# Performance work log

Measured on AMD Instinct MI355X. Metric: run time of the kernel, lower is better.

Reference implementation:

```python
import jax, jax.numpy as jnp
import numpy as np

N, F, H, C = 4096, 128, 32, 205   # nodes, in-features, hidden=32, clusters=ceil(4096/20)
L, T, R = 512, 12, 4              # teams, team size, replaced members per team
EPS_POOL = 1e-15                  # torch_geometric EPS in dense_diff_pool
BN_EPS = 1e-5


def setup_inputs():
    ks = jax.random.split(jax.random.key(0), 12)
    rng = np.random.default_rng(0)
    # distinct node ids per team; replace = first R members, remain = rest
    teams = np.argsort(rng.random((L, N)), axis=1)[:, :T].astype(np.int64)
    g = lambda i, shape, s: jax.random.normal(ks[i], shape, jnp.float32) * s
    D = 2 * H + C  # 269
    return {
        'x': g(0, (N, F), 1.0),
        'adj': jax.random.uniform(ks[1], (1, N, N), jnp.float32),
        'sample_teams': jnp.asarray(teams),
        'sample_replaces': jnp.asarray(teams[:, :R]),
        'W1r': g(2, (F, H), 0.08), 'b1': jnp.zeros((H,), jnp.float32), 'W1root': g(3, (F, H), 0.08),
        'g1': jnp.ones((H,), jnp.float32), 'be1': jnp.zeros((H,), jnp.float32),
        'W2r': g(4, (H, H), 0.17), 'b2': jnp.zeros((H,), jnp.float32), 'W2root': g(5, (H, H), 0.17),
        'g2': jnp.ones((H,), jnp.float32), 'be2': jnp.zeros((H,), jnp.float32),
        'W3r': g(6, (H, C), 0.17), 'b3': jnp.zeros((C,), jnp.float32), 'W3root': g(7, (H, C), 0.17),
        'g3': jnp.ones((C,), jnp.float32), 'be3': jnp.zeros((C,), jnp.float32),
        'Wl1': g(8, (D, C), 0.07), 'bl1': jnp.zeros((C,), jnp.float32),
    }


def _conv(x, adj, Wr, br, Wroot):
    # DenseGraphConv: lin_rel(adj @ x) + lin_root(x)  (lin_root has no bias)
    return jnp.matmul(adj, x) @ Wr + br + x @ Wroot


def _bn(x, gamma, beta):
    # BatchNorm1d in training mode over flattened (B*N, C)
    B, n, c = x.shape
    xf = x.reshape(-1, c)
    m = xf.mean(0)
    v = jnp.mean((xf - m) ** 2, axis=0)  # biased variance, as torch uses for normalization
    return (((xf - m) / jnp.sqrt(v + BN_EPS)) * gamma + beta).reshape(B, n, c)


def _rownorm(a, eps=1e-8):
    n = jnp.linalg.norm(a, axis=1, keepdims=True)
    return a / jnp.maximum(n, eps)


def reference(x, adj, sample_teams, sample_replaces, W1r, b1, W1root, g1, be1,
              W2r, b2, W2root, g2, be2, W3r, b3, W3root, g3, be3, Wl1, bl1):
    # GNN tower (relu before bn, matching self.bn(i, conv(...).relu()))
    x1 = _bn(jax.nn.relu(_conv(x, adj, W1r, b1, W1root)), g1, be1)    # [1,N,H]
    x2 = _bn(jax.nn.relu(_conv(x1, adj, W2r, b2, W2root)), g2, be2)   # [1,N,H]
    x3 = _bn(jax.nn.relu(_conv(x2, adj, W3r, b3, W3root)), g3, be3)   # [1,N,C]
    xcat = jnp.concatenate([x1, x2, x3], axis=-1)                     # [1,N,2H+C]
    s1 = jax.nn.softmax(jax.nn.relu(xcat @ Wl1 + bl1), axis=2)        # [1,N,C]

    # link-prediction style norm: || s1[0] @ s1[0]^T - adj ||_F
    tmp = s1[0] @ s1[0].T - adj                                       # [1,N,N]
    norm = jnp.sqrt(jnp.sum(tmp * tmp))

    # dense_diff_pool entropy loss (it re-softmaxes its input s)
    s2 = jax.nn.softmax(s1, axis=-1)
    e1 = jnp.mean(jnp.sum(-s2 * jnp.log(s2 + EPS_POOL), axis=-1))

    # similarity alignment: only the diagonal of sim_matrix(sim_x_mat, sim_s_mat) is summed
    xn = _rownorm(x)
    sn = _rownorm(s1[0])
    sim_x_mat = xn @ xn.T                                             # [N,N]
    sim_s_mat = sn @ sn.T                                             # [N,N]
    a_n = _rownorm(sim_x_mat)
    b_n = _rownorm(sim_s_mat)
    sim = -jnp.sum(a_n * b_n) / sim_x_mat.shape[0]

    # per-team replace/remain mean-embedding L1 loss (padded segment means)
    emb = xcat[0]                                                     # [N, 2H+C]
    rep = emb[sample_replaces].mean(axis=1)                           # [L, D]
    rem = emb[sample_teams[:, R:]].mean(axis=1)                       # [L, D]
    embedding_loss = jnp.mean(jnp.sum(jnp.abs(rep - rem), axis=-1))

    total_loss = 100.0 * norm + 10.0 * e1 + 100.0 * sim + embedding_loss
    return (s1, norm, e1, sim, total_loss, embedding_loss, emb)
```

## Files before the change

### kernel.cpp

```cpp
#include <hip/hip_runtime.h>
#include <math.h>

#define NN 4096
#define FF 128
#define HH 32
#define CC 205
#define DD 269
#define LL 512
#define TT 12
#define RR 4
#define GP 208
#define DP 288
#define BST 40
#define GTS 224
#define SC(i) ((i) * 32)

typedef __attribute__((ext_vector_type(8))) short bf16x8;
typedef __attribute__((ext_vector_type(4))) float f32x4;
typedef __attribute__((ext_vector_type(8))) unsigned short u16x8;

__device__ __forceinline__ float wave_sum(float v) {
#pragma unroll
  for (int o = 32; o > 0; o >>= 1) v += __shfl_xor(v, o, 64);
  return v;
}
__device__ __forceinline__ float wave_max(float v) {
#pragma unroll
  for (int o = 32; o > 0; o >>= 1) v = fmaxf(v, __shfl_xor(v, o, 64));
  return v;
}
__device__ __forceinline__ unsigned short f2bf(float x) {
  union { float f; unsigned u; } v; v.f = x;
  unsigned r = v.u + 0x7FFFu + ((v.u >> 16) & 1u);
  return (unsigned short)(r >> 16);
}

__global__ __launch_bounds__(256) void k_prep(const float* __restrict__ x,
                                              const float* __restrict__ W1r,
                                              const float* __restrict__ W1root,
                                              const float* __restrict__ Wl1,
                                              unsigned short* __restrict__ mB,
                                              float* __restrict__ rootb,
                                              float* __restrict__ xn,
                                              unsigned short* __restrict__ xnR,
                                              unsigned short* __restrict__ xnB,
                                              unsigned short* __restrict__ Wl1T) {
  __shared__ float sX[32][132];
  __shared__ unsigned short sT[32][34];
  __shared__ unsigned short sT2[FF][34];
  const int tid = threadIdx.x;
  {
    const int i = blockIdx.x * 256 + tid;
    if (i < GP * DP) {
      const int c = i / DP, k = i - c * DP;
      Wl1T[i] = (c < CC && k < DD) ? f2bf(Wl1[(size_t)k * CC + c]) : (unsigned short)0;
    }
  }
  if (blockIdx.x < 128) {
    const int kb = blockIdx.x;
    for (int p = tid; p < 1024; p += 256) {
      const int node = p >> 5, c4 = p & 31;
      const float4 v = *reinterpret_cast<const float4*>(&x[((size_t)(kb * 32 + node)) * FF + c4 * 4]);
      sX[node][c4 * 4 + 0] = v.x; sX[node][c4 * 4 + 1] = v.y;
      sX[node][c4 * 4 + 2] = v.z; sX[node][c4 * 4 + 3] = v.w;
    }
    __syncthreads();
    const int c = tid & 31, g = tid >> 5;
    float a1[4] = {0.f, 0.f, 0.f, 0.f}, a2[4] = {0.f, 0.f, 0.f, 0.f};
    for (int k = 0; k < FF; ++k) {
      const float w1 = W1r[k * HH + c];
      const float w2 = W1root[k * HH + c];
#pragma unroll
      for (int ni = 0; ni < 4; ++ni) {
        const float av = sX[g * 4 + ni][k];
        a1[ni] = fmaf(av, w1, a1[ni]);
        a2[ni] = fmaf(av, w2, a2[ni]);
      }
    }
#pragma unroll
    for (int ni = 0; ni < 4; ++ni) {
      rootb[((size_t)kb * 32 + g * 4 + ni) * HH + c] = a2[ni];
      sT[c][g * 4 + ni] = f2bf(a1[ni]);
    }
    __syncthreads();
    if (tid < 128) {
      const int row = tid >> 2, seg = tid & 3;
      u16x8 v;
#pragma unroll
      for (int j = 0; j < 8; ++j) v[j] = sT[row][seg * 8 + j];
      *reinterpret_cast<u16x8*>(&mB[((size_t)kb * 32 + row) * 32 + seg * 8]) = v;
    }
  } else {
    const int kb = blockIdx.x - 128;
    const int lane = tid & 63;
    const int w = tid >> 6;
#pragma unroll
    for (int i = 0; i < 8; ++i) {
      const int node = w * 8 + i;
      const int row = kb * 32 + node;
      const float v0 = x[(size_t)row * FF + lane];
      const float v1 = x[(size_t)row * FF + 64 + lane];
      const float ss = wave_sum(v0 * v0 + v1 * v1);
      const float n = fmaxf(sqrtf(ss), 1e-8f);
      const float a = v0 / n, b = v1 / n;
      xn[(size_t)row * FF + lane] = a;
      xn[(size_t)row * FF + 64 + lane] = b;
      xnR[(size_t)row * FF + lane] = f2bf(a);
      xnR[(size_t)row * FF + 64 + lane] = f2bf(b);
      sT2[lane][node] = f2bf(a);
      sT2[64 + lane][node] = f2bf(b);
    }
    __syncthreads();
    const int rowc = tid >> 1, seg = (tid & 1) * 16;
    if (rowc < FF) {
      u16x8 a, b;
#pragma unroll
      for (int j = 0; j < 8; ++j) { a[j] = sT2[rowc][seg + j]; b[j] = sT2[rowc][seg + 8 + j]; }
      *reinterpret_cast<u16x8*>(&xnB[((size_t)kb * GP + rowc) * 32 + seg]) = a;
      *reinterpret_cast<u16x8*>(&xnB[((size_t)kb * GP + rowc) * 32 + seg + 8]) = b;
    }
  }
}

__global__ __launch_bounds__(512) void k_conv1(const float* __restrict__ adj,
                                               unsigned short* __restrict__ adj_t,
                                               const unsigned short* __restrict__ mB,
                                               const float* __restrict__ bias,
                                               const float* __restrict__ root,
                                               float* __restrict__ t,
                                               float* __restrict__ colsum,
                                               float* __restrict__ colsq,
                                               float* __restrict__ scalars) {
  __shared__ unsigned short sA[16][520];
  __shared__ float sRed[8][16][33];
  __shared__ float ls[HH], lq[HH];
  __shared__ float redsq[8];
  const int tid = threadIdx.x;
  const int lane = tid & 63;
  const int w = tid >> 6;
  const int l15 = lane & 15;
  const int kgrp = (lane >> 4) * 8;
  const int rb = blockIdx.x;
  const int row0 = rb * 16;
  float adjsq = 0.f;
  f32x4 acc0 = {0.f, 0.f, 0.f, 0.f}, acc1 = {0.f, 0.f, 0.f, 0.f};
  for (int chunk = 0; chunk < 8; ++chunk) {
    const int kbase = chunk * 512;
#pragma unroll
    for (int i = 0; i < 4; ++i) {
      const int fi = i * 512 + tid;
      const int r = fi >> 7;
      const int c4 = fi & 127;
      const size_t goff = (size_t)(row0 + r) * NN + kbase + c4 * 4;
      const float4 v = *reinterpret_cast<const float4*>(&adj[goff]);
      adjsq += v.x * v.x + v.y * v.y + v.z * v.z + v.w * v.w;
      ushort4 h;
      h.x = f2bf(v.x); h.y = f2bf(v.y); h.z = f2bf(v.z); h.w = f2bf(v.w);
      const size_t toff = ((size_t)rb * (NN / 32) + (kbase >> 5) + (c4 >> 3)) * 512 +
                          r * 32 + (c4 & 7) * 4;
      *reinterpret_cast<ushort4*>(&adj_t[toff]) = h;
      *reinterpret_cast<ushort4*>(&sA[r][c4 * 4]) = h;
    }
    __syncthreads();
#pragma unroll
    for (int j = 0; j < 2; ++j) {
      const int ktl = w * 2 + j;
      const bf16x8 a = *reinterpret_cast<const bf16x8*>(&sA[l15][ktl * 32 + kgrp]);
      const size_t boff = (size_t)(chunk * 16 + ktl) * 1024;
      const bf16x8 b0 = *reinterpret_cast<const bf16x8*>(&mB[boff + l15 * 32 + kgrp]);
      const bf16x8 b1v = *reinterpret_cast<const bf16x8*>(&mB[boff + (16 + l15) * 32 + kgrp]);
      acc0 = __builtin_amdgcn_mfma_f32_16x16x32_bf16(a, b0, acc0, 0, 0, 0);
      acc1 = __builtin_amdgcn_mfma_f32_16x16x32_bf16(a, b1v, acc1, 0, 0, 0);
    }
    __syncthreads();
  }
  const int crow = (lane >> 4) * 4;
#pragma unroll
  for (int r = 0; r < 4; ++r) {
    sRed[w][crow + r][l15] = acc0[r];
    sRed[w][crow + r][16 + l15] = acc1[r];
  }
  if (tid < HH) { ls[tid] = 0.f; lq[tid] = 0.f; }
  adjsq = wave_sum(adjsq);
  if (lane == 0) redsq[w] = adjsq;
  __syncthreads();
  {
    const int r = tid >> 5, c = tid & 31;
    float v = 0.f;
#pragma unroll
    for (int i = 0; i < 8; ++i) v += sRed[i][r][c];
    const int n = row0 + r;
    float s = bias[c] + root[(size_t)n * HH + c] + v;
    s = fmaxf(s, 0.f);
    t[(size_t)n * HH + c] = s;
    atomicAdd(&ls[c], s);
    atomicAdd(&lq[c], s * s);
  }
  __syncthreads();
  if (tid < HH) {
    atomicAdd(&colsum[tid * 16], ls[tid]);
    atomicAdd(&colsq[tid * 16], lq[tid]);
  }
  if (tid == 0) {
    float s = 0.f;
#pragma unroll
    for (int i = 0; i < 8; ++i) s += redsq[i];
    atomicAdd(&scalars[SC(1)], s);
  }
}

__global__ __launch_bounds__(512) void k_conv2(const unsigned short* __restrict__ adj_t,
                                               const unsigned short* __restrict__ mB,
                                               const float* __restrict__ bias,
                                               const float* __restrict__ root,
                                               float* __restrict__ t,
                                               float* __restrict__ colsum,
                                               float* __restrict__ colsq) {
  __shared__ float sRed[8][16][33];
  __shared__ float ls[HH], lq[HH];
  const int tid = threadIdx.x;
  const int lane = tid & 63;
  const int w = tid >> 6;
  const int l15 = lane & 15;
  const int kgrp = (lane >> 4) * 8;
  const int rb = blockIdx.x;
  const int row0 = rb * 16;
  const int kb0 = w * 16;
  f32x4 acc0 = {0.f, 0.f, 0.f, 0.f}, acc1 = {0.f, 0.f, 0.f, 0.f};
#pragma unroll
  for (int h = 0; h < 2; ++h) {
    bf16x8 a[8], b0[8], b1v[8];
#pragma unroll
    for (int kt = 0; kt < 8; ++kt) {
      const int kb = kb0 + h * 8 + kt;
      const size_t aoff = ((size_t)rb * (NN / 32) + kb) * 512;
      const size_t boff = (size_t)kb * 1024;
      a[kt] = *reinterpret_cast<const bf16x8*>(&adj_t[aoff + l15 * 32 + kgrp]);
      b0[kt] = *reinterpret_cast<const bf16x8*>(&mB[boff + (size_t)l15 * 32 + kgrp]);
      b1v[kt] = *reinterpret_cast<const bf16x8*>(&mB[boff + (size_t)(16 + l15) * 32 + kgrp]);
    }
#pragma unroll
    for (int kt = 0; kt < 8; ++kt) {
      acc0 = __builtin_amdgcn_mfma_f32_16x16x32_bf16(a[kt], b0[kt], acc0, 0, 0, 0);
      acc1 = __builtin_amdgcn_mfma_f32_16x16x32_bf16(a[kt], b1v[kt], acc1, 0, 0, 0);
    }
  }
  const int crow = (lane >> 4) * 4;
#pragma unroll
  for (int r = 0; r < 4; ++r) {
    sRed[w][crow + r][l15] = acc0[r];
    sRed[w][crow + r][16 + l15] = acc1[r];
  }
  if (tid < HH) { ls[tid] = 0.f; lq[tid] = 0.f; }
  __syncthreads();
  {
    const int r = tid >> 5, c = tid & 31;
    float v = 0.f;
#pragma unroll
    for (int i = 0; i < 8; ++i) v += sRed[i][r][c];
    const int n = row0 + r;
    float s = bias[c] + root[(size_t)n * HH + c] + v;
    s = fmaxf(s, 0.f);
    t[(size_t)n * HH + c] = s;
    atomicAdd(&ls[c], s);
    atomicAdd(&lq[c], s * s);
  }
  __syncthreads();
  if (tid < HH) {
    atomicAdd(&colsum[tid * 16], ls[tid]);
    atomicAdd(&colsq[tid * 16], lq[tid]);
  }
}

__global__ __launch_bounds__(512) void k_conv3(const unsigned short* __restrict__ adj_t,
                                               const unsigned short* __restrict__ x2B,
                                               const float* __restrict__ W3r,
                                               const float* __restrict__ b3,
                                               const float* __restrict__ x2,
                                               const float* __restrict__ W3root,
                                               float* __restrict__ t3,
                                               float* __restrict__ colsum,
                                               float* __restrict__ colsq) {
  __shared__ float sRed[8][16][33];
  __shared__ float sZ[16][33];
  __shared__ float sXr[16][33];
  const int tid = threadIdx.x;
  const int lane = tid & 63;
  const int w = tid >> 6;
  const int l15 = lane & 15;
  const int kgrp = (lane >> 4) * 8;
  const int rb = blockIdx.x;
  const int row0 = rb * 16;
  const int kb0 = w * 16;
  f32x4 acc0 = {0.f, 0.f, 0.f, 0.f}, acc1 = {0.f, 0.f, 0.f, 0.f};
#pragma unroll
  for (int h = 0; h < 2; ++h) {
    bf16x8 a[8], b0[8], b1v[8];
#pragma unroll
    for (int kt = 0; kt < 8; ++kt) {
      const int kb = kb0 + h * 8 + kt;
      const size_t aoff = ((size_t)rb * (NN / 32) + kb) * 512;
      const size_t boff = (size_t)kb * 1024;
      a[kt] = *reinterpret_cast<const bf16x8*>(&adj_t[aoff + l15 * 32 + kgrp]);
      b0[kt] = *reinterpret_cast<const bf16x8*>(&x2B[boff + (size_t)l15 * 32 + kgrp]);
      b1v[kt] = *reinterpret_cast<const bf16x8*>(&x2B[boff + (size_t)(16 + l15) * 32 + kgrp]);
    }
#pragma unroll
    for (int kt = 0; kt < 8; ++kt) {
      acc0 = __builtin_amdgcn_mfma_f32_16x16x32_bf16(a[kt], b0[kt], acc0, 0, 0, 0);
      acc1 = __builtin_amdgcn_mfma_f32_16x16x32_bf16(a[kt], b1v[kt], acc1, 0, 0, 0);
    }
  }
  const int crow = (lane >> 4) * 4;
#pragma unroll
  for (int r = 0; r < 4; ++r) {
    sRed[w][crow + r][l15] = acc0[r];
    sRed[w][crow + r][16 + l15] = acc1[r];
  }
  {
    const int r = tid >> 5, c = tid & 31;
    sXr[r][c] = x2[(size_t)(row0 + r) * HH + c];
  }
  __syncthreads();
  {
    const int r = tid >> 5, c = tid & 31;
    float v = 0.f;
#pragma unroll
    for (int i = 0; i < 8; ++i) v += sRed[i][r][c];
    sZ[r][c] = v;
  }
  __syncthreads();
  const int c = tid;
  if (c >= CC) return;
  float acc[16];
  const float bb = b3[c];
#pragma unroll
  for (int r = 0; r < 16; ++r) acc[r] = bb;
  for (int k = 0; k < 32; ++k) {
    const float w1 = W3r[k * CC + c];
    const float w2 = W3root[k * CC + c];
#pragma unroll
    for (int r = 0; r < 16; ++r) acc[r] += sZ[r][k] * w1 + sXr[r][k] * w2;
  }
  float lsm = 0.f, lqm = 0.f;
#pragma unroll
  for (int r = 0; r < 16; ++r) {
    const float v = fmaxf(acc[r], 0.f);
    t3[(size_t)(row0 + r) * CC + c] = v;
    lsm += v;
    lqm += v * v;
  }
  atomicAdd(&colsum[c * 16], lsm);
  atomicAdd(&colsq[c * 16], lqm);
}

__global__ __launch_bounds__(256) void k_bnproj(const float* __restrict__ t,
                                                const float* __restrict__ colsum,
                                                const float* __restrict__ colsq,
                                                const float* __restrict__ g,
                                                const float* __restrict__ be,
                                                const float* __restrict__ W2r,
                                                const float* __restrict__ W2root,
                                                unsigned short* __restrict__ mB,
                                                float* __restrict__ rootb,
                                                float* __restrict__ emb) {
  __shared__ float sXf[32][33];
  __shared__ unsigned short sT[32][34];
  const int tid = threadIdx.x;
  const int kb = blockIdx.x;
  const int c = tid & 31, gq = tid >> 5;
  const float m = colsum[c * 16] * (1.f / NN);
  const float var = fmaxf(colsq[c * 16] * (1.f / NN) - m * m, 0.f);
  const float Ac = g[c] / sqrtf(var + 1e-5f);
  const float Bc = be[c] - m * Ac;
#pragma unroll
  for (int ni = 0; ni < 4; ++ni) {
    const int n = kb * 32 + gq * 4 + ni;
    const float v = fmaf(Ac, t[(size_t)n * HH + c], Bc);
    emb[(size_t)n * DD + c] = v;
    sXf[gq * 4 + ni][c] = v;
  }
  __syncthreads();
  float a1[4] = {0.f, 0.f, 0.f, 0.f}, a2[4] = {0.f, 0.f, 0.f, 0.f};
  for (int k = 0; k < HH; ++k) {
    const float w1 = W2r[k * HH + c];
    const float w2 = W2root[k * HH + c];
#pragma unroll
    for (int ni = 0; ni < 4; ++ni) {
      const float av = sXf[gq * 4 + ni][k];
      a1[ni] = fmaf(av, w1, a1[ni]);
      a2[ni] = fmaf(av, w2, a2[ni]);
    }
  }
#pragma unroll
  for (int ni = 0; ni < 4; ++ni) {
    rootb[((size_t)kb * 32 + gq * 4 + ni) * HH + c] = a2[ni];
    sT[c][gq * 4 + ni] = f2bf(a1[ni]);
  }
  __syncthreads();
  if (tid < 128) {
    const int row = tid >> 2, seg = tid & 3;
    u16x8 v;
#pragma unroll
    for (int j = 0; j < 8; ++j) v[j] = sT[row][seg * 8 + j];
    *reinterpret_cast<u16x8*>(&mB[((size_t)kb * 32 + row) * 32 + seg * 8]) = v;
  }
}

__global__ __launch_bounds__(256) void k_bnapply32(const float* __restrict__ t,
                                                   const float* __restrict__ colsum,
                                                   const float* __restrict__ colsq,
                                                   const float* __restrict__ g,
                                                   const float* __restrict__ be,
                                                   float* __restrict__ xo,
                                                   float* __restrict__ emb, int embOff,
                                                   unsigned short* __restrict__ xB) {
  __shared__ unsigned short sT[32][34];
  const int tid = threadIdx.x;
  const int kb = blockIdx.x;
  const int c = tid & 31, gq = tid >> 5;
  const float m = colsum[c * 16] * (1.f / NN);
  const float var = fmaxf(colsq[c * 16] * (1.f / NN) - m * m, 0.f);
  const float Ac = g[c] / sqrtf(var + 1e-5f);
  const float Bc = be[c] - m * Ac;
#pragma unroll
  for (int ni = 0; ni < 4; ++ni) {
    const int n = kb * 32 + gq * 4 + ni;
    const float v = fmaf(Ac, t[(size_t)n * HH + c], Bc);
    xo[(size_t)n * HH + c] = v;
    emb[(size_t)n * DD + embOff + c] = v;
    sT[c][gq * 4 + ni] = f2bf(v);
  }
  __syncthreads();
  if (tid < 128) {
    const int row = tid >> 2, seg = tid & 3;
    u16x8 o;
#pragma unroll
    for (int j = 0; j < 8; ++j) o[j] = sT[row][seg * 8 + j];
    *reinterpret_cast<u16x8*>(&xB[((size_t)kb * 32 + row) * 32 + seg * 8]) = o;
  }
}

__global__ __launch_bounds__(256) void k_head(float* __restrict__ emb,
                                              const float* __restrict__ t3,
                                              const float* __restrict__ colsum3,
                                              const float* __restrict__ colsq3,
                                              const float* __restrict__ g3,
                                              const float* __restrict__ be3,
                                              const unsigned short* __restrict__ Wl1T,
                                              const float* __restrict__ bl1,
                                              float* __restrict__ s1,
                                              float* __restrict__ sn,
                                              unsigned short* __restrict__ s1B,
                                              unsigned short* __restrict__ snB,
                                              unsigned short* __restrict__ snR,
                                              float* __restrict__ scalars) {
  __shared__ unsigned short sA[16][296];
  __shared__ float lg[16][212];
  __shared__ unsigned short sTa[16][212];
  __shared__ unsigned short sTb[16][212];
  __shared__ float redE[4];
  const int tid = threadIdx.x;
  const int row0 = blockIdx.x * 16;
  for (int p = tid; p < 16 * 36; p += 256) {
    const int r = p / 36, ch = p - r * 36;
    const int row = row0 + r;
#pragma unroll
    for (int j = 0; j < 8; ++j) {
      const int d = ch * 8 + j;
      float v;
      if (d < 2 * HH) {
        v = emb[(size_t)row * DD + d];
      } else if (d < DD) {
        const int c3 = d - 2 * HH;
        const float m = colsum3[c3 * 16] * (1.f / NN);
        const float var = fmaxf(colsq3[c3 * 16] * (1.f / NN) - m * m, 0.f);
        const float Ac = g3[c3] / sqrtf(var + 1e-5f);
        const float Bc = be3[c3] - m * Ac;
        v = fmaf(Ac, t3[(size_t)row * CC + c3], Bc);
        emb[(size_t)row * DD + d] = v;
      } else {
        v = 0.f;
      }
      sA[r][d] = f2bf(v);
    }
  }
  __syncthreads();
  const int lane = tid & 63;
  const int w = tid >> 6;
  const int l15 = lane & 15;
  const int kgrp = (lane >> 4) * 8;
  {
    f32x4 acc[4];
#pragma unroll
    for (int i = 0; i < 4; ++i) acc[i] = (f32x4){0.f, 0.f, 0.f, 0.f};
#pragma unroll
    for (int i = 0; i < 4; ++i) {
      const int ct = w + i * 4;
      if (ct < 13) {
        const size_t brow = (size_t)(ct * 16 + l15) * DP;
#pragma unroll
        for (int k0 = 0; k0 < DP; k0 += 32) {
          const bf16x8 a = *reinterpret_cast<const bf16x8*>(&sA[l15][k0 + kgrp]);
          const bf16x8 b = *reinterpret_cast<const bf16x8*>(&Wl1T[brow + k0 + kgrp]);
          acc[i] = __builtin_amdgcn_mfma_f32_16x16x32_bf16(a, b, acc[i], 0, 0, 0);
        }
      }
    }
    const int lrow = (lane >> 4) * 4;
#pragma unroll
    for (int i = 0; i < 4; ++i) {
      const int ct = w + i * 4;
      if (ct < 13) {
#pragma unroll
        for (int r = 0; r < 4; ++r) lg[lrow + r][ct * 16 + l15] = acc[i][r];
      }
    }
  }
  __syncthreads();
  const int r0 = w * 4;
  const int c0 = lane * 4;
  const bool active = (c0 < GP);
  float bl[4];
#pragma unroll
  for (int j = 0; j < 4; ++j) bl[j] = (c0 + j < CC) ? bl1[c0 + j] : 0.f;
  float ent_acc = 0.f;
#pragma unroll
  for (int r = 0; r < 4; ++r) {
    const int lr = r0 + r;
    const int row = row0 + lr;
    float lgv[4] = {0.f, 0.f, 0.f, 0.f};
    if (active) {
#pragma unroll
      for (int j = 0; j < 4; ++j) lgv[j] = lg[lr][c0 + j];
    }
    float v[4];
    float ml = -1e30f;
#pragma unroll
    for (int j = 0; j < 4; ++j) {
      const int c = c0 + j;
      v[j] = (c < CC) ? fmaxf(lgv[j] + bl[j], 0.f) : -1e30f;
      ml = fmaxf(ml, v[j]);
    }
    const float m = wave_max(ml);
    float e[4];
    float sl = 0.f;
#pragma unroll
    for (int j = 0; j < 4; ++j) {
      const int c = c0 + j;
      e[j] = (c < CC) ? __expf(v[j] - m) : 0.f;
      sl += e[j];
    }
    const float S = wave_sum(sl);
    const float invS = 1.f / S;
    float p[4];
    float ql = 0.f;
#pragma unroll
    for (int j = 0; j < 4; ++j) {
      p[j] = e[j] * invS;
      ql += p[j] * p[j];
    }
    const float q = wave_sum(ql);
    const float inv = 1.f / fmaxf(sqrtf(q), 1e-8f);
    float m2l = -1e30f;
#pragma unroll
    for (int j = 0; j < 4; ++j) {
      const int c = c0 + j;
      if (c < CC) {
        s1[(size_t)row * CC + c] = p[j];
        sn[(size_t)row * CC + c] = p[j] * inv;
        m2l = fmaxf(m2l, p[j]);
      }
    }
    if (active) {
#pragma unroll
      for (int j = 0; j < 4; ++j) {
        const int c = c0 + j;
        const bool ok = (c < CC);
        sTa[lr][c] = ok ? f2bf(p[j]) : (unsigned short)0;
        sTb[lr][c] = ok ? f2bf(p[j] * inv) : (unsigned short)0;
      }
    }
    if (c0 < GTS) {
      ushort4 o;
      o.x = (c0 + 0 < CC) ? f2bf(p[0] * inv) : (unsigned short)0;
      o.y = (c0 + 1 < CC) ? f2bf(p[1] * inv) : (unsigned short)0;
      o.z = (c0 + 2 < CC) ? f2bf(p[2] * inv) : (unsigned short)0;
      o.w = (c0 + 3 < CC) ? f2bf(p[3] * inv) : (unsigned short)0;
      *reinterpret_cast<ushort4*>(&snR[(size_t)row * GTS + c0]) = o;
    }
    const float m2 = wave_max(m2l);
    float e2[4];
    float s2l = 0.f;
#pragma unroll
    for (int j = 0; j < 4; ++j) {
      const int c = c0 + j;
      e2[j] = (c < CC) ? __expf(p[j] - m2) : 0.f;
      s2l += e2[j];
    }
    const float S2 = wave_sum(s2l);
    const float invS2 = 1.f / S2;
    float tl = 0.f;
#pragma unroll
    for (int j = 0; j < 4; ++j) {
      const int c = c0 + j;
      if (c < CC) {
        const float sp = e2[j] * invS2;
        tl -= sp * logf(sp + 1e-15f);
      }
    }
    ent_acc += tl;
  }
  ent_acc = wave_sum(ent_acc);
  if (lane == 0) redE[w] = ent_acc;
  __syncthreads();
  if (tid == 0) atomicAdd(&scalars[SC(2)], redE[0] + redE[1] + redE[2] + redE[3]);
  if (tid < GP) {
    const int kb = row0 >> 5, no = row0 & 31;
    u16x8 oa0, ob0, oa1, ob1;
#pragma unroll
    for (int r = 0; r < 8; ++r) {
      oa0[r] = sTa[r][tid]; ob0[r] = sTb[r][tid];
      oa1[r] = sTa[8 + r][tid]; ob1[r] = sTb[8 + r][tid];
    }
    *reinterpret_cast<u16x8*>(&s1B[((size_t)kb * GP + tid) * 32 + no]) = oa0;
    *reinterpret_cast<u16x8*>(&s1B[((size_t)kb * GP + tid) * 32 + no + 8]) = oa1;
    *reinterpret_cast<u16x8*>(&snB[((size_t)kb * GP + tid) * 32 + no]) = ob0;
    *reinterpret_cast<u16x8*>(&snB[((size_t)kb * GP + tid) * 32 + no + 8]) = ob1;
  }
}

__global__ __launch_bounds__(512) void k_tail(const unsigned short* __restrict__ adj_t,
                                              const unsigned short* __restrict__ s1B,
                                              const float* __restrict__ s1,
                                              const unsigned short* __restrict__ xnB,
                                              const unsigned short* __restrict__ snB,
                                              unsigned short* __restrict__ GT0,
                                              unsigned short* __restrict__ GxsT,
                                              unsigned short* __restrict__ GsT,
                                              float* __restrict__ scalars) {
  const int tid = threadIdx.x;
  const int lane = tid & 63;
  const int w = tid >> 6;
  const int l15 = lane & 15;
  const int kgrp = (lane >> 4) * 8;
  if (blockIdx.x < 512) {
    __shared__ unsigned short sB[2][13][16][BST];
    __shared__ float red[8];
    const int bx = blockIdx.x & 31;
    const int ky = blockIdx.x >> 5;
    const int rb = bx * 8 + w;
    const int kb0 = ky * 8;
    const int g = lane >> 4;
    const int p0 = tid;
    const int ct0 = p0 >> 6, rr0 = (p0 >> 2) & 15, sg0 = (p0 & 3) * 8;
    const int p1 = tid + 512;
    const bool v1 = (p1 < 832);
    const int ct1 = p1 >> 6, rr1 = (p1 >> 2) & 15, sg1 = (p1 & 3) * 8;
    f32x4 acc[13];
#pragma unroll
    for (int ct = 0; ct < 13; ++ct) acc[ct] = (f32x4){0.f, 0.f, 0.f, 0.f};
    u16x8 st0, st1;
    st0 = *reinterpret_cast<const u16x8*>(&s1B[((size_t)kb0 * GP + ct0 * 16 + rr0) * 32 + sg0]);
    if (v1) st1 = *reinterpret_cast<const u16x8*>(&s1B[((size_t)kb0 * GP + ct1 * 16 + rr1) * 32 + sg1]);
    *reinterpret_cast<u16x8*>(&sB[0][ct0][rr0][sg0]) = st0;
    if (v1) *reinterpret_cast<u16x8*>(&sB[0][ct1][rr1][sg1]) = st1;
    __syncthreads();
    bf16x8 a = *reinterpret_cast<const bf16x8*>(
        &adj_t[((size_t)rb * (NN / 32) + kb0) * 512 + l15 * 32 + kgrp]);
    for (int kt = 0; kt < 8; ++kt) {
      const int cur = kt & 1;
      if (kt < 7) {
        const size_t kb = kb0 + kt + 1;
        st0 = *reinterpret_cast<const u16x8*>(&s1B[(kb * GP + ct0 * 16 + rr0) * 32 + sg0]);
        if (v1) st1 = *reinterpret_cast<const u16x8*>(&s1B[(kb * GP + ct1 * 16 + rr1) * 32 + sg1]);
      }
      bf16x8 a_next = a;
      if (kt < 7)
        a_next = *reinterpret_cast<const bf16x8*>(
            &adj_t[((size_t)rb * (NN / 32) + kb0 + kt + 1) * 512 + l15 * 32 + kgrp]);
#pragma unroll
      for (int ct = 0; ct < 13; ++ct) {
        const bf16x8 b = *reinterpret_cast<const bf16x8*>(&sB[cur][ct][l15][kgrp]);
        acc[ct] = __builtin_amdgcn_mfma_f32_16x16x32_bf16(a, b, acc[ct], 0, 0, 0);
      }
      if (kt < 7) {
        *reinterpret_cast<u16x8*>(&sB[cur ^ 1][ct0][rr0][sg0]) = st0;
        if (v1) *reinterpret_cast<u16x8*>(&sB[cur ^ 1][ct1][rr1][sg1]) = st1;
      }
      __syncthreads();
      a = a_next;
    }
    const int rout = rb * 16 + g * 4;
    float sc = 0.f;
#pragma unroll
    for (int ct = 0; ct < 13; ++ct) {
      const int col = ct * 16 + l15;
      if (col < CC) {
#pragma unroll
        for (int r = 0; r < 4; ++r)
          sc = fmaf(acc[ct][r], s1[(size_t)(rout + r) * CC + col], sc);
      }
    }
    sc = wave_sum(sc);
    if (lane == 0) red[w] = sc;
    __syncthreads();
    if (tid == 0) {
      float s = 0.f;
#pragma unroll
      for (int i = 0; i < 8; ++i) s += red[i];
      atomicAdd(&scalars[SC(0)], s);
    }
  } else {
    __shared__ float redg[8][16][17];
    __shared__ float redq[8];
    const int gb = blockIdx.x - 512;
    const int gid = gb / 169;
    const int rem = gb - gid * 169;
    const int tp = (rem % 13) * 16;
    const int tq = (rem / 13) * 16;
    const unsigned short *PT, *QT;
    unsigned short* GTout = nullptr;
    if (gid == 0)      { PT = xnB; QT = xnB; GTout = GT0;  if (tp >= FF || tq >= FF) return; }
    else if (gid == 1) { PT = xnB; QT = snB; GTout = GxsT; if (tp >= FF) return; }
    else if (gid == 2) { PT = snB; QT = snB; GTout = GsT; }
    else               { PT = s1B; QT = s1B; }
    f32x4 acc = {0.f, 0.f, 0.f, 0.f};
#pragma unroll 4
    for (int kt = 0; kt < 16; ++kt) {
      const int kb = w * 16 + kt;
      const bf16x8 a = *reinterpret_cast<const bf16x8*>(&PT[((size_t)kb * GP + tp + l15) * 32 + kgrp]);
      const bf16x8 b = *reinterpret_cast<const bf16x8*>(&QT[((size_t)kb * GP + tq + l15) * 32 + kgrp]);
      acc = __builtin_amdgcn_mfma_f32_16x16x32_bf16(a, b, acc, 0, 0, 0);
    }
    const int crow = (lane >> 4) * 4;
#pragma unroll
    for (int r = 0; r < 4; ++r) redg[w][crow + r][l15] = acc[r];
    __syncthreads();
    const int rr = tid >> 4, cc = tid & 15;
    if (gid == 3) {
      float q = 0.f;
      if (tid < 256) {
        float v = 0.f;
#pragma unroll
        for (int i = 0; i < 8; ++i) v += redg[i][rr][cc];
        q = v * v;
      }
      q = wave_sum(q);
      if (lane == 0) redq[w] = q;
      __syncthreads();
      if (tid == 0) {
        float s = 0.f;
#pragma unroll
        for (int i = 0; i < 8; ++i) s += redq[i];
        atomicAdd(&scalars[SC(5)], s);
      }
    } else {
      if (tid < 256) {
        float vt = 0.f;
#pragma unroll
        for (int i = 0; i < 8; ++i) vt += redg[i][cc][rr];
        GTout[(size_t)(tq + rr) * GTS + (tp + cc)] = f2bf(vt);
      }
    }
  }
}

__global__ __launch_bounds__(256) void k_rowsim(const unsigned short* __restrict__ xnR,
                                                const unsigned short* __restrict__ snR,
                                                const unsigned short* __restrict__ GT0,
                                                const unsigned short* __restrict__ GxsT,
                                                const unsigned short* __restrict__ GsT,
                                                const float* __restrict__ xn,
                                                const float* __restrict__ sn,
                                                float* __restrict__ scalars) {
  __shared__ unsigned short sX[16][136];
  __shared__ unsigned short sS[16][232];
  __shared__ float sH1[16][132];
  __shared__ float sU[16][212];
  __shared__ float sH2[16][212];
  __shared__ float redb[4];
  const int tid = threadIdx.x;
  const int row0 = blockIdx.x * 16;
  for (int p = tid; p < 16 * 16; p += 256) {
    const int r = p >> 4, ch = p & 15;
    *reinterpret_cast<u16x8*>(&sX[r][ch * 8]) =
        *reinterpret_cast<const u16x8*>(&xnR[(size_t)(row0 + r) * FF + ch * 8]);
  }
  for (int p = tid; p < 16 * 28; p += 256) {
    const int r = p / 28, ch = p - r * 28;
    *reinterpret_cast<u16x8*>(&sS[r][ch * 8]) =
        *reinterpret_cast<const u16x8*>(&snR[(size_t)(row0 + r) * GTS + ch * 8]);
  }
  __syncthreads();
  const int lane = tid & 63;
  const int w = tid >> 6;
  const int l15 = lane & 15;
  const int kgrp = (lane >> 4) * 8;
  const int lrow = (lane >> 4) * 4;
#pragma unroll
  for (int i = 0; i < 2; ++i) {
    const int ct = w + i * 4;
    f32x4 acc = {0.f, 0.f, 0.f, 0.f};
    const size_t brow = (size_t)(ct * 16 + l15) * GTS;
#pragma unroll
    for (int k0 = 0; k0 < FF; k0 += 32) {
      const bf16x8 a = *reinterpret_cast<const bf16x8*>(&sX[l15][k0 + kgrp]);
      const bf16x8 b = *reinterpret_cast<const bf16x8*>(&GT0[brow + k0 + kgrp]);
      acc = __builtin_amdgcn_mfma_f32_16x16x32_bf16(a, b, acc, 0, 0, 0);
    }
#pragma unroll
    for (int r = 0; r < 4; ++r) sH1[lrow + r][ct * 16 + l15] = acc[r];
  }
#pragma unroll
  for (int i = 0; i < 4; ++i) {
    const int ct = w + i * 4;
    if (ct < 13) {
      f32x4 acc = {0.f, 0.f, 0.f, 0.f};
      const size_t brow = (size_t)(ct * 16 + l15) * GTS;
#pragma unroll
      for (int k0 = 0; k0 < FF; k0 += 32) {
        const bf16x8 a = *reinterpret_cast<const bf16x8*>(&sX[l15][k0 + kgrp]);
        const bf16x8 b = *reinterpret_cast<const bf16x8*>(&GxsT[brow + k0 + kgrp]);
        acc = __builtin_amdgcn_mfma_f32_16x16x32_bf16(a, b, acc, 0, 0, 0);
      }
#pragma unroll
      for (int r = 0; r < 4; ++r) sU[lrow + r][ct * 16 + l15] = acc[r];
    }
  }
#pragma unroll
  for (int i = 0; i < 4; ++i) {
    const int ct = w + i * 4;
    if (ct < 13) {
      f32x4 acc = {0.f, 0.f, 0.f, 0.f};
      const size_t brow = (size_t)(ct * 16 + l15) * GTS;
#pragma unroll
      for (int k0 = 0; k0 < GTS; k0 += 32) {
        const bf16x8 a = *reinterpret_cast<const bf16x8*>(&sS[l15][k0 + kgrp]);
        const bf16x8 b = *reinterpret_cast<const bf16x8*>(&GsT[brow + k0 + kgrp]);
        acc = __builtin_amdgcn_mfma_f32_16x16x32_bf16(a, b, acc, 0, 0, 0);
      }
#pragma unroll
      for (int r = 0; r < 4; ++r) sH2[lrow + r][ct * 16 + l15] = acc[r];
    }
  }
  __syncthreads();
  float acc_sim = 0.f;
#pragma unroll
  for (int r = 0; r < 4; ++r) {
    const int lr = w * 4 + r;
    const int row = row0 + lr;
    float suu = 0.f, suv = 0.f, svv = 0.f;
#pragma unroll
    for (int c0 = 0; c0 < FF; c0 += 64) {
      suu = fmaf(xn[(size_t)row * FF + c0 + lane], sH1[lr][c0 + lane], suu);
    }
    for (int cb = lane; cb < CC; cb += 64) {
      const float sv = sn[(size_t)row * CC + cb];
      suv = fmaf(sU[lr][cb], sv, suv);
      svv = fmaf(sH2[lr][cb], sv, svv);
    }
    suu = wave_sum(suu);
    suv = wave_sum(suv);
    svv = wave_sum(svv);
    if (lane == 0) acc_sim += suv / sqrtf(suu * svv);
  }
  if (lane == 0) redb[w] = acc_sim;
  __syncthreads();
  if (tid == 0) atomicAdd(&scalars[SC(3)], redb[0] + redb[1] + redb[2] + redb[3]);
}

__global__ __launch_bounds__(256) void k_teams(const float* __restrict__ emb,
                                               const int* __restrict__ teams,
                                               const int* __restrict__ reps,
                                               float* __restrict__ scalars,
                                               unsigned int* __restrict__ ticket,
                                               float* __restrict__ outsc) {
  __shared__ float red[4];
  const int tid = threadIdx.x;
  const int team = blockIdx.x;
  float part = 0.f;
  for (int d = tid; d < DD; d += 256) {
    float a = 0.f, b = 0.f;
#pragma unroll
    for (int m = 0; m < RR; ++m) a += emb[(size_t)reps[team * RR + m] * DD + d];
#pragma unroll
    for (int m = RR; m < TT; ++m) b += emb[(size_t)teams[team * TT + m] * DD + d];
    part += fabsf(a * (1.f / RR) - b * (1.f / (TT - RR)));
  }
  part = wave_sum(part);
  if ((tid & 63) == 0) red[tid >> 6] = part;
  __syncthreads();
  if (tid == 0) {
    atomicAdd(&scalars[SC(4)], red[0] + red[1] + red[2] + red[3]);
    __threadfence();
    const unsigned int old = atomicAdd(ticket, 1u);
    if (old == (unsigned int)(LL - 1)) {
      const float trSAS = atomicAdd(&scalars[SC(0)], 0.f);
      const float adjsq = atomicAdd(&scalars[SC(1)], 0.f);
      const float ent   = atomicAdd(&scalars[SC(2)], 0.f);
      const float simS  = atomicAdd(&scalars[SC(3)], 0.f);
      const float embS  = atomicAdd(&scalars[SC(4)], 0.f);
      const float sumP2 = atomicAdd(&scalars[SC(5)], 0.f);
      const float normsq = fmaxf(sumP2 - 2.f * trSAS + adjsq, 0.f);
      const float norm = sqrtf(normsq);
      const float e1 = ent * (1.f / NN);
      const float sim = -simS * (1.f / NN);
      const float embl = embS * (1.f / LL);
      outsc[0] = norm;
      outsc[1] = e1;
      outsc[2] = sim;
      outsc[3] = 100.f * norm + 10.f * e1 + 100.f * sim + embl;
      outsc[4] = embl;
    }
  }
}

extern "C" void kernel_launch(void* const* d_in, const int* in_sizes, int n_in,
                              void* d_out, int out_size, void* d_ws, size_t ws_size,
                              hipStream_t stream) {
  const float* x      = (const float*)d_in[0];
  const float* adj    = (const float*)d_in[1];
  const int*   teams  = (const int*)d_in[2];
  const int*   reps   = (const int*)d_in[3];
  const float* W1r    = (const float*)d_in[4];
  const float* b1     = (const float*)d_in[5];
  const float* W1root = (const float*)d_in[6];
  const float* g1     = (const float*)d_in[7];
  const float* be1    = (const float*)d_in[8];
  const float* W2r    = (const float*)d_in[9];
  const float* b2     = (const float*)d_in[10];
  const float* W2root = (const float*)d_in[11];
  const float* g2     = (const float*)d_in[12];
  const float* be2    = (const float*)d_in[13];
  const float* W3r    = (const float*)d_in[14];
  const float* b3     = (const float*)d_in[15];
  const float* W3root = (const float*)d_in[16];
  const float* g3     = (const float*)d_in[17];
  const float* be3    = (const float*)d_in[18];
  const float* Wl1    = (const float*)d_in[19];
  const float* bl1    = (const float*)d_in[20];

  char* wp = (char*)d_ws;
  auto alloc = [&](size_t bytes) { char* p = wp; wp += (bytes + 255) & ~(size_t)255; return p; };
  unsigned short* adj_t = (unsigned short*)alloc((size_t)NN * NN * 2);
  unsigned short* mB    = (unsigned short*)alloc((size_t)HH * NN * 2);
  unsigned short* x2B   = (unsigned short*)alloc((size_t)HH * NN * 2);
  unsigned short* s1B   = (unsigned short*)alloc((size_t)GP * NN * 2);
  unsigned short* snB   = (unsigned short*)alloc((size_t)GP * NN * 2);
  unsigned short* Wl1T  = (unsigned short*)alloc((size_t)GP * DP * 2);
  unsigned short* xnR   = (unsigned short*)alloc((size_t)NN * FF * 2);
  unsigned short* snR   = (unsigned short*)alloc((size_t)NN * GTS * 2);
  float* rootb  = (float*)alloc((size_t)NN * HH * 4);
  float* t      = (float*)alloc((size_t)NN * HH * 4);
  float* x2     = (float*)alloc((size_t)NN * HH * 4);
  float* t3     = (float*)alloc((size_t)NN * CC * 4);
  float* sn     = (float*)alloc((size_t)NN * CC * 4);
  float* xn     = (float*)alloc((size_t)NN * FF * 4);
  float* scalars = (float*)alloc(256 * 4);
  float* colsum1 = (float*)alloc(512 * 4);
  float* colsq1  = (float*)alloc(512 * 4);
  float* colsum2 = (float*)alloc(512 * 4);
  float* colsq2  = (float*)alloc(512 * 4);
  float* colsum3 = (float*)alloc(4096 * 4);
  float* colsq3  = (float*)alloc(4096 * 4);
  unsigned short* GTall = (unsigned short*)alloc((size_t)3 * GP * GTS * 2);
  unsigned short* xnB   = (unsigned short*)alloc((size_t)GP * NN * 2);
  char* zero_end = wp;
  unsigned short* GT0   = GTall;
  unsigned short* GxsT  = GTall + (size_t)GP * GTS;
  unsigned short* GsT   = GTall + (size_t)2 * GP * GTS;
  unsigned int* ticket = (unsigned int*)&scalars[SC(6)];
  (void)ws_size; (void)in_sizes; (void)n_in; (void)out_size;

  float* out   = (float*)d_out;
  float* s1    = out;
  float* outsc = out + (size_t)NN * CC;
  float* emb   = out + (size_t)NN * CC + 5;

  hipMemsetAsync(scalars, 0, (size_t)(zero_end - (char*)scalars), stream);

  k_prep<<<256, 256, 0, stream>>>(x, W1r, W1root, Wl1, mB, rootb, xn, xnR, xnB, Wl1T);

  k_conv1<<<256, 512, 0, stream>>>(adj, adj_t, mB, b1, rootb, t, colsum1, colsq1, scalars);
  k_bnproj<<<NN / 32, 256, 0, stream>>>(t, colsum1, colsq1, g1, be1, W2r, W2root, mB, rootb, emb);

  k_conv2<<<256, 512, 0, stream>>>(adj_t, mB, b2, rootb, t, colsum2, colsq2);
  k_bnapply32<<<NN / 32, 256, 0, stream>>>(t, colsum2, colsq2, g2, be2, x2, emb, HH, x2B);

  k_conv3<<<256, 512, 0, stream>>>(adj_t, x2B, W3r, b3, x2, W3root, t3, colsum3, colsq3);

  k_head<<<NN / 16, 256, 0, stream>>>(emb, t3, colsum3, colsq3, g3, be3, Wl1T, bl1,
                                      s1, sn, s1B, snB, snR, scalars);

  k_tail<<<512 + 676, 512, 0, stream>>>(adj_t, s1B, s1, xnB, snB, GT0, GxsT, GsT, scalars);

  k_rowsim<<<NN / 16, 256, 0, stream>>>(xnR, snR, GT0, GxsT, GsT, xn, sn, scalars);
  k_teams<<<LL, 256, 0, stream>>>(emb, teams, reps, scalars, ticket, outsc);
}
```

Measured before the change: 189.8 us.

## Fold memset into prep, merge rowsim and teams kernels, prefetch adj in conv1

Drops the hipMemsetAsync by having k_prep zero the scalar/stat and GT buffers, which are regrouped so they are contiguous. Merges k_rowsim and k_teams into one k_finloss launch of 768 blocks, with the completion ticket now counting all of them. In conv1, the next adj chunk is software-prefetched into registers before the MFMA stage of the current chunk, overlapping the global load with compute. The cost is higher register pressure and relying on k_prep's zeroing finishing before later kernels read those buffers.

```diff
diff --git a/kernel.cpp b/kernel.cpp
--- a/kernel.cpp
+++ b/kernel.cpp
@@ -13,7 +13,10 @@
 #define DP 288
 #define BST 40
 #define GTS 224
+#define NFIN 768
 #define SC(i) ((i) * 32)
+#define ZSTATS_N 10496
+#define ZGT_N 69888
 
 typedef __attribute__((ext_vector_type(8))) short bf16x8;
 typedef __attribute__((ext_vector_type(4))) float f32x4;
@@ -44,16 +47,20 @@
                                               float* __restrict__ xn,
                                               unsigned short* __restrict__ xnR,
                                               unsigned short* __restrict__ xnB,
-                                              unsigned short* __restrict__ Wl1T) {
+                                              unsigned short* __restrict__ Wl1T,
+                                              float* __restrict__ zstats,
+                                              unsigned int* __restrict__ zgt) {
   __shared__ float sX[32][132];
   __shared__ unsigned short sT[32][34];
   __shared__ unsigned short sT2[FF][34];
   const int tid = threadIdx.x;
   {
-    const int i = blockIdx.x * 256 + tid;
-    if (i < GP * DP) {
-      const int c = i / DP, k = i - c * DP;
-      Wl1T[i] = (c < CC && k < DD) ? f2bf(Wl1[(size_t)k * CC + c]) : (unsigned short)0;
+    const int gidx = blockIdx.x * 256 + tid;
+    if (gidx < ZSTATS_N) zstats[gidx] = 0.f;
+    for (int i = gidx; i < ZGT_N; i += 65536) zgt[i] = 0u;
+    if (gidx < GP * DP) {
+      const int c = gidx / DP, k = gidx - c * DP;
+      Wl1T[gidx] = (c < CC && k < DD) ? f2bf(Wl1[(size_t)k * CC + c]) : (unsigned short)0;
     }
   }
   if (blockIdx.x < 128) {
@@ -144,24 +151,34 @@
   const int row0 = rb * 16;
   float adjsq = 0.f;
   f32x4 acc0 = {0.f, 0.f, 0.f, 0.f}, acc1 = {0.f, 0.f, 0.f, 0.f};
+  const int fr[4] = {(0 * 512 + tid) >> 7, (1 * 512 + tid) >> 7, (2 * 512 + tid) >> 7,
+                     (3 * 512 + tid) >> 7};
+  const int fc[4] = {(0 * 512 + tid) & 127, (1 * 512 + tid) & 127, (2 * 512 + tid) & 127,
+                     (3 * 512 + tid) & 127};
+  float4 v[4];
+#pragma unroll
+  for (int i = 0; i < 4; ++i)
+    v[i] = *reinterpret_cast<const float4*>(&adj[(size_t)(row0 + fr[i]) * NN + fc[i] * 4]);
   for (int chunk = 0; chunk < 8; ++chunk) {
     const int kbase = chunk * 512;
 #pragma unroll
     for (int i = 0; i < 4; ++i) {
-      const int fi = i * 512 + tid;
-      const int r = fi >> 7;
-      const int c4 = fi & 127;
-      const size_t goff = (size_t)(row0 + r) * NN + kbase + c4 * 4;
-      const float4 v = *reinterpret_cast<const float4*>(&adj[goff]);
-      adjsq += v.x * v.x + v.y * v.y + v.z * v.z + v.w * v.w;
+      const float4 vv = v[i];
+      adjsq += vv.x * vv.x + vv.y * vv.y + vv.z * vv.z + vv.w * vv.w;
       ushort4 h;
-      h.x = f2bf(v.x); h.y = f2bf(v.y); h.z = f2bf(v.z); h.w = f2bf(v.w);
-      const size_t toff = ((size_t)rb * (NN / 32) + (kbase >> 5) + (c4 >> 3)) * 512 +
-                          r * 32 + (c4 & 7) * 4;
+      h.x = f2bf(vv.x); h.y = f2bf(vv.y); h.z = f2bf(vv.z); h.w = f2bf(vv.w);
+      const size_t toff = ((size_t)rb * (NN / 32) + (kbase >> 5) + (fc[i] >> 3)) * 512 +
+                          fr[i] * 32 + (fc[i] & 7) * 4;
       *reinterpret_cast<ushort4*>(&adj_t[toff]) = h;
-      *reinterpret_cast<ushort4*>(&sA[r][c4 * 4]) = h;
-    }
-    __syncthreads();
+      *reinterpret_cast<ushort4*>(&sA[fr[i]][fc[i] * 4]) = h;
+    }
+    __syncthreads();
+    if (chunk < 7) {
+      const int kn = kbase + 512;
+#pragma unroll
+      for (int i = 0; i < 4; ++i)
+        v[i] = *reinterpret_cast<const float4*>(&adj[(size_t)(row0 + fr[i]) * NN + kn + fc[i] * 4]);
+    }
 #pragma unroll
     for (int j = 0; j < 2; ++j) {
       const int ktl = w * 2 + j;
@@ -186,11 +203,11 @@
   __syncthreads();
   {
     const int r = tid >> 5, c = tid & 31;
-    float v = 0.f;
-#pragma unroll
-    for (int i = 0; i < 8; ++i) v += sRed[i][r][c];
+    float vv = 0.f;
+#pragma unroll
+    for (int i = 0; i < 8; ++i) vv += sRed[i][r][c];
     const int n = row0 + r;
-    float s = bias[c] + root[(size_t)n * HH + c] + v;
+    float s = bias[c] + root[(size_t)n * HH + c] + vv;
     s = fmaxf(s, 0.f);
     t[(size_t)n * HH + c] = s;
     atomicAdd(&ls[c], s);
@@ -319,7 +336,7 @@
   }
   {
     const int r = tid >> 5, c = tid & 31;
-    sXr[r][c] = x2[(size_t)(row0 + r) * HH + c];
+    if (tid < 512) sXr[r][c] = x2[(size_t)(row0 + r) * HH + c];
   }
   __syncthreads();
   {
@@ -766,136 +783,136 @@
   }
 }
 
-__global__ __launch_bounds__(256) void k_rowsim(const unsigned short* __restrict__ xnR,
-                                                const unsigned short* __restrict__ snR,
-                                                const unsigned short* __restrict__ GT0,
-                                                const unsigned short* __restrict__ GxsT,
-                                                const unsigned short* __restrict__ GsT,
-                                                const float* __restrict__ xn,
-                                                const float* __restrict__ sn,
-                                                float* __restrict__ scalars) {
-  __shared__ unsigned short sX[16][136];
-  __shared__ unsigned short sS[16][232];
-  __shared__ float sH1[16][132];
-  __shared__ float sU[16][212];
-  __shared__ float sH2[16][212];
-  __shared__ float redb[4];
+__global__ __launch_bounds__(256) void k_finloss(const unsigned short* __restrict__ xnR,
+                                                 const unsigned short* __restrict__ snR,
+                                                 const unsigned short* __restrict__ GT0,
+                                                 const unsigned short* __restrict__ GxsT,
+                                                 const unsigned short* __restrict__ GsT,
+                                                 const float* __restrict__ xn,
+                                                 const float* __restrict__ sn,
+                                                 const float* __restrict__ emb,
+                                                 const int* __restrict__ teams,
+                                                 const int* __restrict__ reps,
+                                                 float* __restrict__ scalars,
+                                                 unsigned int* __restrict__ ticket,
+                                                 float* __restrict__ outsc) {
+  __shared__ __align__(16) char smem[47424];
   const int tid = threadIdx.x;
-  const int row0 = blockIdx.x * 16;
-  for (int p = tid; p < 16 * 16; p += 256) {
-    const int r = p >> 4, ch = p & 15;
-    *reinterpret_cast<u16x8*>(&sX[r][ch * 8]) =
-        *reinterpret_cast<const u16x8*>(&xnR[(size_t)(row0 + r) * FF + ch * 8]);
-  }
-  for (int p = tid; p < 16 * 28; p += 256) {
-    const int r = p / 28, ch = p - r * 28;
-    *reinterpret_cast<u16x8*>(&sS[r][ch * 8]) =
-        *reinterpret_cast<const u16x8*>(&snR[(size_t)(row0 + r) * GTS + ch * 8]);
-  }
-  __syncthreads();
-  const int lane = tid & 63;
-  const int w = tid >> 6;
-  const int l15 = lane & 15;
-  const int kgrp = (lane >> 4) * 8;
-  const int lrow = (lane >> 4) * 4;
-#pragma unroll
-  for (int i = 0; i < 2; ++i) {
-    const int ct = w + i * 4;
-    f32x4 acc = {0.f, 0.f, 0.f, 0.f};
-    const size_t brow = (size_t)(ct * 16 + l15) * GTS;
-#pragma unroll
-    for (int k0 = 0; k0 < FF; k0 += 32) {
-      const bf16x8 a = *reinterpret_cast<const bf16x8*>(&sX[l15][k0 + kgrp]);
-      const bf16x8 b = *reinterpret_cast<const bf16x8*>(&GT0[brow + k0 + kgrp]);
-      acc = __builtin_amdgcn_mfma_f32_16x16x32_bf16(a, b, acc, 0, 0, 0);
-    }
-#pragma unroll
-    for (int r = 0; r < 4; ++r) sH1[lrow + r][ct * 16 + l15] = acc[r];
-  }
-#pragma unroll
-  for (int i = 0; i < 4; ++i) {
-    const int ct = w + i * 4;
-    if (ct < 13) {
+  if (blockIdx.x < 256) {
+    unsigned short (*sX)[136] = (unsigned short(*)[136])(smem);
+    unsigned short (*sS)[232] = (unsigned short(*)[232])(smem + 4352);
+    float (*sH1)[132] = (float(*)[132])(smem + 11776);
+    float (*sU)[212] = (float(*)[212])(smem + 20224);
+    float (*sH2)[212] = (float(*)[212])(smem + 33792);
+    float* redb = (float*)(smem + 47360);
+    const int row0 = blockIdx.x * 16;
+    for (int p = tid; p < 16 * 16; p += 256) {
+      const int r = p >> 4, ch = p & 15;
+      *reinterpret_cast<u16x8*>(&sX[r][ch * 8]) =
+          *reinterpret_cast<const u16x8*>(&xnR[(size_t)(row0 + r) * FF + ch * 8]);
+    }
+    for (int p = tid; p < 16 * 28; p += 256) {
+      const int r = p / 28, ch = p - r * 28;
+      *reinterpret_cast<u16x8*>(&sS[r][ch * 8]) =
+          *reinterpret_cast<const u16x8*>(&snR[(size_t)(row0 + r) * GTS + ch * 8]);
+    }
+    __syncthreads();
+    const int lane = tid & 63;
+    const int w = tid >> 6;
+    const int l15 = lane & 15;
+    const int kgrp = (lane >> 4) * 8;
+    const int lrow = (lane >> 4) * 4;
+#pragma unroll
+    for (int i = 0; i < 2; ++i) {
+      const int ct = w + i * 4;
       f32x4 acc = {0.f, 0.f, 0.f, 0.f};
       const size_t brow = (size_t)(ct * 16 + l15) * GTS;
 #pragma unroll
       for (int k0 = 0; k0 < FF; k0 += 32) {
         const bf16x8 a = *reinterpret_cast<const bf16x8*>(&sX[l15][k0 + kgrp]);
-        const bf16x8 b = *reinterpret_cast<const bf16x8*>(&GxsT[brow + k0 + kgrp]);
+        const bf16x8 b = *reinterpret_cast<const bf16x8*>(&GT0[brow + k0 + kgrp]);
         acc = __builtin_amdgcn_mfma_f32_16x16x32_bf16(a, b, acc, 0, 0, 0);
       }
 #pragma unroll
-      for (int r = 0; r < 4; ++r) sU[lrow + r][ct * 16 + l15] = acc[r];
-    }
-  }
-#pragma unroll
-  for (int i = 0; i < 4; ++i) {
-    const int ct = w + i * 4;
-    if (ct < 13) {
-      f32x4 acc = {0.f, 0.f, 0.f, 0.f};
-      const size_t brow = (size_t)(ct * 16 + l15) * GTS;
-#pragma unroll
-      for (int k0 = 0; k0 < GTS; k0 += 32) {
-        const bf16x8 a = *reinterpret_cast<const bf16x8*>(&sS[l15][k0 + kgrp]);
-        const bf16x8 b = *reinterpret_cast<const bf16x8*>(&GsT[brow + k0 + kgrp]);
-        acc = __builtin_amdgcn_mfma_f32_16x16x32_bf16(a, b, acc, 0, 0, 0);
-      }
-#pragma unroll
-      for (int r = 0; r < 4; ++r) sH2[lrow + r][ct * 16 + l15] = acc[r];
-    }
-  }
-  __syncthreads();
-  float acc_sim = 0.f;
-#pragma unroll
-  for (int r = 0; r < 4; ++r) {
-    const int lr = w * 4 + r;
-    const int row = row0 + lr;
-    float suu = 0.f, suv = 0.f, svv = 0.f;
-#pragma unroll
-    for (int c0 = 0; c0 < FF; c0 += 64) {
-      suu = fmaf(xn[(size_t)row * FF + c0 + lane], sH1[lr][c0 + lane], suu);
-    }
-    for (int cb = lane; cb < CC; cb += 64) {
-      const float sv = sn[(size_t)row * CC + cb];
-      suv = fmaf(sU[lr][cb], sv, suv);
-      svv = fmaf(sH2[lr][cb], sv, svv);
-    }
-    suu = wave_sum(suu);
-    suv = wave_sum(suv);
-    svv = wave_sum(svv);
-    if (lane == 0) acc_sim += suv / sqrtf(suu * svv);
-  }
-  if (lane == 0) redb[w] = acc_sim;
-  __syncthreads();
-  if (tid == 0) atomicAdd(&scalars[SC(3)], redb[0] + redb[1] + redb[2] + redb[3]);
-}
-
-__global__ __launch_bounds__(256) void k_teams(const float* __restrict__ emb,
-                                               const int* __restrict__ teams,
-                                               const int* __restrict__ reps,
-                                               float* __restrict__ scalars,
-                                               unsigned int* __restrict__ ticket,
-                                               float* __restrict__ outsc) {
-  __shared__ float red[4];
-  const int tid = threadIdx.x;
-  const int team = blockIdx.x;
-  float part = 0.f;
-  for (int d = tid; d < DD; d += 256) {
-    float a = 0.f, b = 0.f;
-#pragma unroll
-    for (int m = 0; m < RR; ++m) a += emb[(size_t)reps[team * RR + m] * DD + d];
-#pragma unroll
-    for (int m = RR; m < TT; ++m) b += emb[(size_t)teams[team * TT + m] * DD + d];
-    part += fabsf(a * (1.f / RR) - b * (1.f / (TT - RR)));
-  }
-  part = wave_sum(part);
-  if ((tid & 63) == 0) red[tid >> 6] = part;
-  __syncthreads();
+      for (int r = 0; r < 4; ++r) sH1[lrow + r][ct * 16 + l15] = acc[r];
+    }
+#pragma unroll
+    for (int i = 0; i < 4; ++i) {
+      const int ct = w + i * 4;
+      if (ct < 13) {
+        f32x4 acc = {0.f, 0.f, 0.f, 0.f};
+        const size_t brow = (size_t)(ct * 16 + l15) * GTS;
+#pragma unroll
+        for (int k0 = 0; k0 < FF; k0 += 32) {
+          const bf16x8 a = *reinterpret_cast<const bf16x8*>(&sX[l15][k0 + kgrp]);
+          const bf16x8 b = *reinterpret_cast<const bf16x8*>(&GxsT[brow + k0 + kgrp]);
+          acc = __builtin_amdgcn_mfma_f32_16x16x32_bf16(a, b, acc, 0, 0, 0);
+        }
+#pragma unroll
+        for (int r = 0; r < 4; ++r) sU[lrow + r][ct * 16 + l15] = acc[r];
+      }
+    }
+#pragma unroll
+    for (int i = 0; i < 4; ++i) {
+      const int ct = w + i * 4;
+      if (ct < 13) {
+        f32x4 acc = {0.f, 0.f, 0.f, 0.f};
+        const size_t brow = (size_t)(ct * 16 + l15) * GTS;
+#pragma unroll
+        for (int k0 = 0; k0 < GTS; k0 += 32) {
+          const bf16x8 a = *reinterpret_cast<const bf16x8*>(&sS[l15][k0 + kgrp]);
+          const bf16x8 b = *reinterpret_cast<const bf16x8*>(&GsT[brow + k0 + kgrp]);
+          acc = __builtin_amdgcn_mfma_f32_16x16x32_bf16(a, b, acc, 0, 0, 0);
+        }
+#pragma unroll
+        for (int r = 0; r < 4; ++r) sH2[lrow + r][ct * 16 + l15] = acc[r];
+      }
+    }
+    __syncthreads();
+    float acc_sim = 0.f;
+#pragma unroll
+    for (int r = 0; r < 4; ++r) {
+      const int lr = w * 4 + r;
+      const int row = row0 + lr;
+      float suu = 0.f, suv = 0.f, svv = 0.f;
+#pragma unroll
+      for (int c0 = 0; c0 < FF; c0 += 64) {
+        suu = fmaf(xn[(size_t)row * FF + c0 + lane], sH1[lr][c0 + lane], suu);
+      }
+      for (int cb = lane; cb < CC; cb += 64) {
+        const float sv = sn[(size_t)row * CC + cb];
+        suv = fmaf(sU[lr][cb], sv, suv);
+        svv = fmaf(sH2[lr][cb], sv, svv);
+      }
+      suu = wave_sum(suu);
+      suv = wave_sum(suv);
+      svv = wave_sum(svv);
+      if (lane == 0) acc_sim += suv / sqrtf(suu * svv);
+    }
+    if (lane == 0) redb[w] = acc_sim;
+    __syncthreads();
+    if (tid == 0) atomicAdd(&scalars[SC(3)], redb[0] + redb[1] + redb[2] + redb[3]);
+  } else {
+    float* red = (float*)smem;
+    const int team = blockIdx.x - 256;
+    float part = 0.f;
+    for (int d = tid; d < DD; d += 256) {
+      float a = 0.f, b = 0.f;
+#pragma unroll
+      for (int m = 0; m < RR; ++m) a += emb[(size_t)reps[team * RR + m] * DD + d];
+#pragma unroll
+      for (int m = RR; m < TT; ++m) b += emb[(size_t)teams[team * TT + m] * DD + d];
+      part += fabsf(a * (1.f / RR) - b * (1.f / (TT - RR)));
+    }
+    part = wave_sum(part);
+    if ((tid & 63) == 0) red[tid >> 6] = part;
+    __syncthreads();
+    if (tid == 0) atomicAdd(&scalars[SC(4)], red[0] + red[1] + red[2] + red[3]);
+  }
   if (tid == 0) {
-    atomicAdd(&scalars[SC(4)], red[0] + red[1] + red[2] + red[3]);
     __threadfence();
     const unsigned int old = atomicAdd(ticket, 1u);
-    if (old == (unsigned int)(LL - 1)) {
+    if (old == (unsigned int)(NFIN - 1)) {
       const float trSAS = atomicAdd(&scalars[SC(0)], 0.f);
       const float adjsq = atomicAdd(&scalars[SC(1)], 0.f);
       const float ent   = atomicAdd(&scalars[SC(2)], 0.f);
@@ -957,6 +974,7 @@
   float* t3     = (float*)alloc((size_t)NN * CC * 4);
   float* sn     = (float*)alloc((size_t)NN * CC * 4);
   float* xn     = (float*)alloc((size_t)NN * FF * 4);
+  unsigned short* xnB   = (unsigned short*)alloc((size_t)GP * NN * 2);
   float* scalars = (float*)alloc(256 * 4);
   float* colsum1 = (float*)alloc(512 * 4);
   float* colsq1  = (float*)alloc(512 * 4);
@@ -965,8 +983,6 @@
   float* colsum3 = (float*)alloc(4096 * 4);
   float* colsq3  = (float*)alloc(4096 * 4);
   unsigned short* GTall = (unsigned short*)alloc((size_t)3 * GP * GTS * 2);
-  unsigned short* xnB   = (unsigned short*)alloc((size_t)GP * NN * 2);
-  char* zero_end = wp;
   unsigned short* GT0   = GTall;
   unsigned short* GxsT  = GTall + (size_t)GP * GTS;
   unsigned short* GsT   = GTall + (size_t)2 * GP * GTS;
@@ -978,9 +994,8 @@
   float* outsc = out + (size_t)NN * CC;
   float* emb   = out + (size_t)NN * CC + 5;
 
-  hipMemsetAsync(scalars, 0, (size_t)(zero_end - (char*)scalars), stream);
-
-  k_prep<<<256, 256, 0, stream>>>(x, W1r, W1root, Wl1, mB, rootb, xn, xnR, xnB, Wl1T);
+  k_prep<<<256, 256, 0, stream>>>(x, W1r, W1root, Wl1, mB, rootb, xn, xnR, xnB, Wl1T,
+                                  scalars, (unsigned int*)GTall);
 
   k_conv1<<<256, 512, 0, stream>>>(adj, adj_t, mB, b1, rootb, t, colsum1, colsq1, scalars);
   k_bnproj<<<NN / 32, 256, 0, stream>>>(t, colsum1, colsq1, g1, be1, W2r, W2root, mB, rootb, emb);
@@ -995,6 +1010,6 @@
 
   k_tail<<<512 + 676, 512, 0, stream>>>(adj_t, s1B, s1, xnB, snB, GT0, GxsT, GsT, scalars);
 
-  k_rowsim<<<NN / 16, 256, 0, stream>>>(xnR, snR, GT0, GxsT, GsT, xn, sn, scalars);
-  k_teams<<<LL, 256, 0, stream>>>(emb, teams, reps, scalars, ticket, outsc);
-}
+  k_finloss<<<NFIN, 256, 0, stream>>>(xnR, snR, GT0, GxsT, GsT, xn, sn, emb, teams, reps,
+                                      scalars, ticket, outsc);
+}
```

Result: faster. 182.0 us, median of 2 (-4.1%).
